# Kernel tuning notes

Measured on AMD Instinct MI355X. Metric: run time of the kernel, lower is better.

## Reference

```python
import jax, jax.numpy as jnp
import numpy as np

N_NODES = 50000
N_EDGES = 800000
F_NODE = 64
F_EDGE = 64
HIDDEN = 128


def setup_inputs() -> dict:
    key = jax.random.key(0)
    ks = jax.random.split(key, 12)
    glorot = lambda k, shape: jax.random.normal(k, shape, jnp.float32) * (2.0 / (shape[0] + shape[1])) ** 0.5
    return {
        "x": jax.random.normal(ks[0], (N_NODES, F_NODE), jnp.float32),
        "edge_index": jax.random.randint(ks[1], (2, N_EDGES), 0, N_NODES, jnp.int64),
        "edge_attr": jax.random.normal(ks[2], (N_EDGES, F_EDGE), jnp.float32),
        # edge model: MLP(concat(x_src, x_dst, edge_attr)) -> new edge_attr
        "We1": glorot(ks[3], (2 * F_NODE + F_EDGE, HIDDEN)),
        "be1": jnp.zeros((HIDDEN,), jnp.float32),
        "We2": glorot(ks[4], (HIDDEN, F_EDGE)),
        "be2": jnp.zeros((F_EDGE,), jnp.float32),
        # node model: MLP(concat(x, mean_{e: dst==i} edge_attr_e)) -> new x
        "Wn1": glorot(ks[5], (F_NODE + F_EDGE, HIDDEN)),
        "bn1": jnp.zeros((HIDDEN,), jnp.float32),
        "Wn2": glorot(ks[6], (HIDDEN, F_NODE)),
        "bn2": jnp.zeros((F_NODE,), jnp.float32),
    }


def _mlp(h, W1, b1, W2, b2):
    return jax.nn.relu(h @ W1 + b1) @ W2 + b2


def reference(x, edge_index, edge_attr, We1, be1, We2, be2, Wn1, bn1, Wn2, bn2):
    row, col = edge_index[0], edge_index[1]
    # edge model: message on each edge  [E, 2F+Fe] -> [E, Fe]
    edge_in = jnp.concatenate([x[row], x[col], edge_attr], axis=-1)
    edge_attr = _mlp(edge_in, We1, be1, We2, be2)
    # node model: mean-aggregate incoming messages at dst (col), then MLP
    agg = jax.ops.segment_sum(edge_attr, col, num_segments=N_NODES)
    cnt = jax.ops.segment_sum(jnp.ones((edge_attr.shape[0],), x.dtype), col, num_segments=N_NODES)
    agg = agg / jnp.maximum(cnt, 1.0)[:, None]
    node_in = jnp.concatenate([x, agg], axis=-1)
    x = _mlp(node_in, Wn1, bn1, Wn2, bn2)
    return (x, edge_attr)
```

## Files before the change

### kernel.cpp

```cpp
#include <hip/hip_runtime.h>


typedef __attribute__((ext_vector_type(8))) short bf16x8;
typedef __attribute__((ext_vector_type(4))) float f4;
typedef __attribute__((ext_vector_type(8))) unsigned short us8;
typedef __attribute__((ext_vector_type(4))) unsigned short us4;

constexpr int NN  = 50000;
constexpr int NE  = 800000;
constexpr int FN  = 64;
constexpr int FE  = 64;
constexpr int HID = 128;
constexpr int K1  = 2 * FN + FE;
constexpr int K2  = FN + FE;

__device__ __forceinline__ float b2f(unsigned short u) {
  union { unsigned int i; float f; } v; v.i = ((unsigned int)u) << 16; return v.f;
}
__device__ __forceinline__ unsigned short f2b(float f) {
  union { float f; unsigned int i; } v; v.f = f;
  unsigned int r = v.i + 0x7FFFu + ((v.i >> 16) & 1u);
  return (unsigned short)(r >> 16);
}
__device__ __forceinline__ void cvt16(const f4* __restrict__ p, unsigned short* dst) {
  f4 a = p[0], b = p[1], c = p[2], d = p[3];
  us8 o0, o1;
#pragma unroll
  for (int j = 0; j < 4; j++) {
    o0[j] = f2b(a[j]); o0[4 + j] = f2b(b[j]);
    o1[j] = f2b(c[j]); o1[4 + j] = f2b(d[j]);
  }
  *(us8*)dst = o0; *(us8*)(dst + 8) = o1;
}
__device__ __forceinline__ f4 MF(bf16x8 a, bf16x8 b, f4 c) {
  return __builtin_amdgcn_mfma_f32_16x16x32_bf16(a, b, c, 0, 0, 0);
}
__device__ __forceinline__ void pk_atomic_add_bf16(unsigned short* addr, unsigned int data) {
  asm volatile("global_atomic_pk_add_bf16 %0, %1, off" :: "v"(addr), "v"(data) : "memory");
}

__global__ void zeroi_kernel(unsigned int* __restrict__ p, int n) {
  int i = blockIdx.x * 256 + threadIdx.x;
  if (i < n) p[i] = 0u;
}

__global__ void cnt_kernel(const int* __restrict__ ei, float* __restrict__ cnt) {
  int e = blockIdx.x * 256 + threadIdx.x;
  if (e < NE) atomicAdd(&cnt[ei[NE + e]], 1.0f);
}

__global__ void pack_w(const float* __restrict__ W, unsigned short* __restrict__ P,
                       int N, int total) {
  int idx = blockIdx.x * 256 + threadIdx.x;
  if (idx >= total) return;
  const int l  = idx & 63;
  const int nt = (idx >> 6) % (N >> 4);
  const int s  = idx / ((N >> 4) << 6);
  const int col = nt * 16 + (l & 15);
  const int k0  = s * 32 + (l >> 4) * 8;
  us8 o;
#pragma unroll
  for (int j = 0; j < 8; j++) o[j] = f2b(W[(size_t)(k0 + j) * N + col]);
  *(us8*)(P + (size_t)idx * 8) = o;
}

__global__ __launch_bounds__(256) void edge_mlp(
    const float* __restrict__ x, const int* __restrict__ ei,
    const float* __restrict__ ea,
    const unsigned short* __restrict__ P1, const float* __restrict__ be1,
    const unsigned short* __restrict__ P2, const float* __restrict__ be2,
    float* __restrict__ eout, unsigned short* __restrict__ aggb) {
  __shared__ unsigned short sA[64][200];
  __shared__ int sC[64];
  unsigned short (*sH)[136] = (unsigned short(*)[136])&sA[0][0];
  const int tid = threadIdx.x;
  const int e0  = blockIdx.x * 64;

  {
    const int el = tid >> 2, q = tid & 3, ge = e0 + el;
    const int r = ei[ge], c = ei[NE + ge];
    if (q == 0) sC[el] = c;
    cvt16((const f4*)(x + (size_t)r * FN + q * 16), &sA[el][q * 16]);
    cvt16((const f4*)(x + (size_t)c * FN + q * 16), &sA[el][64 + q * 16]);
    cvt16((const f4*)(ea + (size_t)ge * FE + q * 16), &sA[el][128 + q * 16]);
  }
  __syncthreads();

  const int wave = tid >> 6, lane = tid & 63;
  const int mrow = lane & 15, kq = lane >> 4;

  f4 acc[4][2];
#pragma unroll
  for (int m = 0; m < 4; m++) { acc[m][0] = (f4)0.f; acc[m][1] = (f4)0.f; }
  const int nt0 = wave * 2;
#pragma unroll
  for (int s = 0; s < 6; s++) {
    bf16x8 b0 = *(const bf16x8*)(P1 + (((size_t)s * 8 + nt0)     * 64 + lane) * 8);
    bf16x8 b1 = *(const bf16x8*)(P1 + (((size_t)s * 8 + nt0 + 1) * 64 + lane) * 8);
#pragma unroll
    for (int m = 0; m < 4; m++) {
      bf16x8 a = *(const bf16x8*)&sA[m * 16 + mrow][s * 32 + kq * 8];
      acc[m][0] = MF(a, b0, acc[m][0]);
      acc[m][1] = MF(a, b1, acc[m][1]);
    }
  }
  __syncthreads();

  {
    const int c0 = nt0 * 16 + mrow, c1 = c0 + 16;
    const float bb0 = be1[c0], bb1 = be1[c1];
    const int rb = kq * 4;
#pragma unroll
    for (int m = 0; m < 4; m++)
#pragma unroll
      for (int i = 0; i < 4; i++) {
        sH[m * 16 + rb + i][c0] = f2b(fmaxf(acc[m][0][i] + bb0, 0.f));
        sH[m * 16 + rb + i][c1] = f2b(fmaxf(acc[m][1][i] + bb1, 0.f));
      }
  }
  __syncthreads();

  f4 a2[4];
#pragma unroll
  for (int m = 0; m < 4; m++) a2[m] = (f4)0.f;
#pragma unroll
  for (int s = 0; s < 4; s++) {
    bf16x8 b = *(const bf16x8*)(P2 + (((size_t)s * 4 + wave) * 64 + lane) * 8);
#pragma unroll
    for (int m = 0; m < 4; m++) {
      bf16x8 a = *(const bf16x8*)&sH[m * 16 + mrow][s * 32 + kq * 8];
      a2[m] = MF(a, b, a2[m]);
    }
  }
  {
    const int col = wave * 16 + mrow;
    const float bb = be2[col];
    const int rb = kq * 4;
    const bool even = ((lane & 1) == 0);
#pragma unroll
    for (int m = 0; m < 4; m++)
#pragma unroll
      for (int i = 0; i < 4; i++) {
        const int er = m * 16 + rb + i;
        const float v = a2[m][i] + bb;
        eout[(size_t)(e0 + er) * FE + col] = v;
        const float vp = __shfl_xor(v, 1);
        if (even) {
          const unsigned int pk =
              (unsigned int)f2b(v) | ((unsigned int)f2b(vp) << 16);
          pk_atomic_add_bf16(aggb + ((size_t)sC[er] * FE + col), pk);
        }
      }
  }
}

__global__ __launch_bounds__(256) void node_mlp(
    const float* __restrict__ x, const unsigned short* __restrict__ aggb,
    const float* __restrict__ cnt,
    const unsigned short* __restrict__ P1, const float* __restrict__ bn1,
    const unsigned short* __restrict__ P2, const float* __restrict__ bn2,
    float* __restrict__ xout) {
  __shared__ unsigned short sA[64][136];
  unsigned short (*sH)[136] = (unsigned short(*)[136])&sA[0][0];
  const int tid = threadIdx.x;
  const int n0  = blockIdx.x * 64;

  {
    const int nl = tid >> 2, q = tid & 3;
    const int gn = n0 + nl;
    if (gn < NN) {
      if (q < 2) {
        cvt16((const f4*)(x + (size_t)gn * FN + q * 32),      &sA[nl][q * 32]);
        cvt16((const f4*)(x + (size_t)gn * FN + q * 32 + 16), &sA[nl][q * 32 + 16]);
      } else {
        const float inv = 1.0f / fmaxf(cnt[gn], 1.0f);
        const int q2 = q - 2;
        const us8* pa = (const us8*)(aggb + (size_t)gn * FE + q2 * 32);
#pragma unroll
        for (int seg = 0; seg < 4; seg++) {
          us8 a = pa[seg];
          us8 o;
#pragma unroll
          for (int j = 0; j < 8; j++) o[j] = f2b(b2f(a[j]) * inv);
          *(us8*)&sA[nl][64 + q2 * 32 + seg * 8] = o;
        }
      }
    } else {
      us8 z = (us8)0;
#pragma unroll
      for (int sgi = 0; sgi < 4; sgi++) *(us8*)&sA[nl][q * 32 + sgi * 8] = z;
    }
  }
  __syncthreads();

  const int wave = tid >> 6, lane = tid & 63;
  const int mrow = lane & 15, kq = lane >> 4;

  f4 acc[4][2];
#pragma unroll
  for (int m = 0; m < 4; m++) { acc[m][0] = (f4)0.f; acc[m][1] = (f4)0.f; }
  const int nt0 = wave * 2;
#pragma unroll
  for (int s = 0; s < 4; s++) {
    bf16x8 b0 = *(const bf16x8*)(P1 + (((size_t)s * 8 + nt0)     * 64 + lane) * 8);
    bf16x8 b1 = *(const bf16x8*)(P1 + (((size_t)s * 8 + nt0 + 1) * 64 + lane) * 8);
#pragma unroll
    for (int m = 0; m < 4; m++) {
      bf16x8 a = *(const bf16x8*)&sA[m * 16 + mrow][s * 32 + kq * 8];
      acc[m][0] = MF(a, b0, acc[m][0]);
      acc[m][1] = MF(a, b1, acc[m][1]);
    }
  }
  __syncthreads();

  {
    const int c0 = nt0 * 16 + mrow, c1 = c0 + 16;
    const float bb0 = bn1[c0], bb1 = bn1[c1];
    const int rb = kq * 4;
#pragma unroll
    for (int m = 0; m < 4; m++)
#pragma unroll
      for (int i = 0; i < 4; i++) {
        sH[m * 16 + rb + i][c0] = f2b(fmaxf(acc[m][0][i] + bb0, 0.f));
        sH[m * 16 + rb + i][c1] = f2b(fmaxf(acc[m][1][i] + bb1, 0.f));
      }
  }
  __syncthreads();

  f4 a2[4];
#pragma unroll
  for (int m = 0; m < 4; m++) a2[m] = (f4)0.f;
#pragma unroll
  for (int s = 0; s < 4; s++) {
    bf16x8 b = *(const bf16x8*)(P2 + (((size_t)s * 4 + wave) * 64 + lane) * 8);
#pragma unroll
    for (int m = 0; m < 4; m++) {
      bf16x8 a = *(const bf16x8*)&sH[m * 16 + mrow][s * 32 + kq * 8];
      a2[m] = MF(a, b, a2[m]);
    }
  }
  {
    const int col = wave * 16 + mrow;
    const float bb = bn2[col];
    const int rb = kq * 4;
#pragma unroll
    for (int m = 0; m < 4; m++)
#pragma unroll
      for (int i = 0; i < 4; i++) {
        const int gn = n0 + m * 16 + rb + i;
        if (gn < NN) xout[(size_t)gn * FN + col] = a2[m][i] + bb;
      }
  }
}

extern "C" void kernel_launch(void* const* d_in, const int* in_sizes, int n_in,
                              void* d_out, int out_size, void* d_ws, size_t ws_size,
                              hipStream_t stream) {
  if (n_in != 11) return;
  if (in_sizes[0] != NN * FN) return;
  if (in_sizes[1] != 2 * NE) return;
  if (in_sizes[2] != NE * FE) return;
  if (out_size != NN * FN + NE * FE) return;
  if (ws_size < (size_t)NN * FE * 2 + (size_t)NN * 4 + 114688) return;

  const float* x   = (const float*)d_in[0];
  const int*   ei  = (const int*)d_in[1];
  const float* ea  = (const float*)d_in[2];
  const float* We1 = (const float*)d_in[3];
  const float* be1 = (const float*)d_in[4];
  const float* We2 = (const float*)d_in[5];
  const float* be2 = (const float*)d_in[6];
  const float* Wn1 = (const float*)d_in[7];
  const float* bn1 = (const float*)d_in[8];
  const float* Wn2 = (const float*)d_in[9];
  const float* bn2 = (const float*)d_in[10];

  float* xout = (float*)d_out;
  float* eout = xout + (size_t)NN * FN;

  unsigned short* aggb = (unsigned short*)d_ws;
  float* cnt = (float*)(aggb + (size_t)NN * FE);
  unsigned short* P   = (unsigned short*)(cnt + NN);
  unsigned short* Pe1 = P;
  unsigned short* Pe2 = P + 24576;
  unsigned short* Pn1 = P + 32768;
  unsigned short* Pn2 = P + 49152;

  const int zi = (NN * FE) / 2 + NN;
  zeroi_kernel<<<(zi + 255) / 256, 256, 0, stream>>>((unsigned int*)d_ws, zi);
  cnt_kernel<<<(NE + 255) / 256, 256, 0, stream>>>(ei, cnt);
  pack_w<<<(3072 + 255) / 256, 256, 0, stream>>>(We1, Pe1, HID, 3072);
  pack_w<<<(1024 + 255) / 256, 256, 0, stream>>>(We2, Pe2, FE, 1024);
  pack_w<<<(2048 + 255) / 256, 256, 0, stream>>>(Wn1, Pn1, HID, 2048);
  pack_w<<<(1024 + 255) / 256, 256, 0, stream>>>(Wn2, Pn2, FN, 1024);
  edge_mlp<<<NE / 64, 256, 0, stream>>>(x, ei, ea, Pe1, be1, Pe2, be2, eout, aggb);
  node_mlp<<<(NN + 63) / 64, 256, 0, stream>>>(x, aggb, cnt, Pn1, bn1, Pn2, bn2, xout);
}
```

Baseline: 304.7 us.

## Make edge MLP wave-independent with per-wave 16-edge tiles, removing block barriers

Each wave now owns 16 edges with its own LDS slice and computes all output column tiles itself, instead of the block sharing 64 edges across 4 waves that each compute a subset of columns. This removes the three __syncthreads barriers and replaces them with an lgkmcnt wait plus a scheduling barrier. The cost is that every wave reloads the full packed weight matrices from global memory or cache (4x more weight traffic per block), and the accumulator register count grows.

```diff
diff --git a/kernel.cpp b/kernel.cpp
--- a/kernel.cpp
+++ b/kernel.cpp
@@ -70,87 +70,84 @@
     const unsigned short* __restrict__ P1, const float* __restrict__ be1,
     const unsigned short* __restrict__ P2, const float* __restrict__ be2,
     float* __restrict__ eout, unsigned short* __restrict__ aggb) {
-  __shared__ unsigned short sA[64][200];
+  __shared__ unsigned short sW[4][16][200];
   __shared__ int sC[64];
-  unsigned short (*sH)[136] = (unsigned short(*)[136])&sA[0][0];
-  const int tid = threadIdx.x;
-  const int e0  = blockIdx.x * 64;
-
-  {
-    const int el = tid >> 2, q = tid & 3, ge = e0 + el;
+  const int tid  = threadIdx.x;
+  const int wave = tid >> 6, lane = tid & 63;
+  const int e0   = blockIdx.x * 64 + wave * 16;
+  unsigned short (*sA)[200] = sW[wave];
+  unsigned short (*sH)[136] = (unsigned short(*)[136])&sW[wave][0][0];
+
+  {
+    const int el = lane >> 2, q = lane & 3, ge = e0 + el;
     const int r = ei[ge], c = ei[NE + ge];
-    if (q == 0) sC[el] = c;
+    if (q == 0) sC[wave * 16 + el] = c;
     cvt16((const f4*)(x + (size_t)r * FN + q * 16), &sA[el][q * 16]);
     cvt16((const f4*)(x + (size_t)c * FN + q * 16), &sA[el][64 + q * 16]);
     cvt16((const f4*)(ea + (size_t)ge * FE + q * 16), &sA[el][128 + q * 16]);
   }
-  __syncthreads();
-
-  const int wave = tid >> 6, lane = tid & 63;
+
   const int mrow = lane & 15, kq = lane >> 4;
 
-  f4 acc[4][2];
-#pragma unroll
-  for (int m = 0; m < 4; m++) { acc[m][0] = (f4)0.f; acc[m][1] = (f4)0.f; }
-  const int nt0 = wave * 2;
-#pragma unroll
+  f4 acc1[8];
+#pragma unroll
+  for (int nt = 0; nt < 8; nt++) acc1[nt] = (f4)0.f;
   for (int s = 0; s < 6; s++) {
-    bf16x8 b0 = *(const bf16x8*)(P1 + (((size_t)s * 8 + nt0)     * 64 + lane) * 8);
-    bf16x8 b1 = *(const bf16x8*)(P1 + (((size_t)s * 8 + nt0 + 1) * 64 + lane) * 8);
-#pragma unroll
-    for (int m = 0; m < 4; m++) {
-      bf16x8 a = *(const bf16x8*)&sA[m * 16 + mrow][s * 32 + kq * 8];
-      acc[m][0] = MF(a, b0, acc[m][0]);
-      acc[m][1] = MF(a, b1, acc[m][1]);
-    }
-  }
-  __syncthreads();
-
-  {
-    const int c0 = nt0 * 16 + mrow, c1 = c0 + 16;
-    const float bb0 = be1[c0], bb1 = be1[c1];
-    const int rb = kq * 4;
-#pragma unroll
-    for (int m = 0; m < 4; m++)
+    bf16x8 a = *(const bf16x8*)&sA[mrow][s * 32 + kq * 8];
+#pragma unroll
+    for (int nt = 0; nt < 8; nt++) {
+      bf16x8 b = *(const bf16x8*)(P1 + (((size_t)s * 8 + nt) * 64 + lane) * 8);
+      acc1[nt] = MF(a, b, acc1[nt]);
+    }
+  }
+
+  asm volatile("s_waitcnt lgkmcnt(0)" ::: "memory");
+  __builtin_amdgcn_sched_barrier(0);
+
+  {
+    const int rb = kq * 4;
+#pragma unroll
+    for (int nt = 0; nt < 8; nt++) {
+      const int col = nt * 16 + mrow;
+      const float bb = be1[col];
+#pragma unroll
+      for (int i = 0; i < 4; i++)
+        sH[rb + i][col] = f2b(fmaxf(acc1[nt][i] + bb, 0.f));
+    }
+  }
+
+  f4 acc2[4];
+#pragma unroll
+  for (int nt = 0; nt < 4; nt++) acc2[nt] = (f4)0.f;
+  for (int s = 0; s < 4; s++) {
+    bf16x8 a = *(const bf16x8*)&sH[mrow][s * 32 + kq * 8];
+#pragma unroll
+    for (int nt = 0; nt < 4; nt++) {
+      bf16x8 b = *(const bf16x8*)(P2 + (((size_t)s * 4 + nt) * 64 + lane) * 8);
+      acc2[nt] = MF(a, b, acc2[nt]);
+    }
+  }
+
+  {
+    const int rb = kq * 4;
+    const bool even = ((lane & 1) == 0);
+#pragma unroll
+    for (int nt = 0; nt < 4; nt++) {
+      const int col = nt * 16 + mrow;
+      const float bb = be2[col];
 #pragma unroll
       for (int i = 0; i < 4; i++) {
-        sH[m * 16 + rb + i][c0] = f2b(fmaxf(acc[m][0][i] + bb0, 0.f));
-        sH[m * 16 + rb + i][c1] = f2b(fmaxf(acc[m][1][i] + bb1, 0.f));
-      }
-  }
-  __syncthreads();
-
-  f4 a2[4];
-#pragma unroll
-  for (int m = 0; m < 4; m++) a2[m] = (f4)0.f;
-#pragma unroll
-  for (int s = 0; s < 4; s++) {
-    bf16x8 b = *(const bf16x8*)(P2 + (((size_t)s * 4 + wave) * 64 + lane) * 8);
-#pragma unroll
-    for (int m = 0; m < 4; m++) {
-      bf16x8 a = *(const bf16x8*)&sH[m * 16 + mrow][s * 32 + kq * 8];
-      a2[m] = MF(a, b, a2[m]);
-    }
-  }
-  {
-    const int col = wave * 16 + mrow;
-    const float bb = be2[col];
-    const int rb = kq * 4;
-    const bool even = ((lane & 1) == 0);
-#pragma unroll
-    for (int m = 0; m < 4; m++)
-#pragma unroll
-      for (int i = 0; i < 4; i++) {
-        const int er = m * 16 + rb + i;
-        const float v = a2[m][i] + bb;
-        eout[(size_t)(e0 + er) * FE + col] = v;
+        const int erl = rb + i;
+        const float v = acc2[nt][i] + bb;
+        eout[(size_t)(e0 + erl) * FE + col] = v;
         const float vp = __shfl_xor(v, 1);
         if (even) {
           const unsigned int pk =
               (unsigned int)f2b(v) | ((unsigned int)f2b(vp) << 16);
-          pk_atomic_add_bf16(aggb + ((size_t)sC[er] * FE + col), pk);
+          pk_atomic_add_bf16(aggb + ((size_t)sC[wave * 16 + erl] * FE + col), pk);
         }
       }
+    }
   }
 }
 
```

New measurement: 361.9 us. 1.19x slower.

## Make edge MLP persistent with register-prefetched gathers for the next tile

Applied to the files above, without the earlier changes.

The edge kernel now runs a fixed grid of 2500 blocks, each handling 5 tiles of 64 edges. While the MFMA work for the current tile runs, the x/edge_attr gathers for the next tile and the edge indices for the tile after that are loaded into registers. This hides gather latency behind compute and cuts block launch overhead. The cost is higher register pressure, which can lower occupancy, and fewer blocks to spread across CUs.

```diff
diff --git a/kernel.cpp b/kernel.cpp
--- a/kernel.cpp
+++ b/kernel.cpp
@@ -4,7 +4,6 @@
 typedef __attribute__((ext_vector_type(8))) short bf16x8;
 typedef __attribute__((ext_vector_type(4))) float f4;
 typedef __attribute__((ext_vector_type(8))) unsigned short us8;
-typedef __attribute__((ext_vector_type(4))) unsigned short us4;
 
 constexpr int NN  = 50000;
 constexpr int NE  = 800000;
@@ -13,6 +12,8 @@
 constexpr int HID = 128;
 constexpr int K1  = 2 * FN + FE;
 constexpr int K2  = FN + FE;
+constexpr int GRID_E    = 2500;
+constexpr int TPB_TILES = 5;
 
 __device__ __forceinline__ float b2f(unsigned short u) {
   union { unsigned int i; float f; } v; v.i = ((unsigned int)u) << 16; return v.f;
@@ -22,15 +23,22 @@
   unsigned int r = v.i + 0x7FFFu + ((v.i >> 16) & 1u);
   return (unsigned short)(r >> 16);
 }
+__device__ __forceinline__ void st16(const f4* r, unsigned short* dst) {
+  us8 o0, o1;
+#pragma unroll
+  for (int j = 0; j < 4; j++) {
+    o0[j] = f2b(r[0][j]); o0[4 + j] = f2b(r[1][j]);
+    o1[j] = f2b(r[2][j]); o1[4 + j] = f2b(r[3][j]);
+  }
+  *(us8*)dst = o0; *(us8*)(dst + 8) = o1;
+}
+__device__ __forceinline__ void ld16(const float* p, f4* r) {
+  const f4* pp = (const f4*)p;
+  r[0] = pp[0]; r[1] = pp[1]; r[2] = pp[2]; r[3] = pp[3];
+}
 __device__ __forceinline__ void cvt16(const f4* __restrict__ p, unsigned short* dst) {
-  f4 a = p[0], b = p[1], c = p[2], d = p[3];
-  us8 o0, o1;
-#pragma unroll
-  for (int j = 0; j < 4; j++) {
-    o0[j] = f2b(a[j]); o0[4 + j] = f2b(b[j]);
-    o1[j] = f2b(c[j]); o1[4 + j] = f2b(d[j]);
-  }
-  *(us8*)dst = o0; *(us8*)(dst + 8) = o1;
+  f4 r[4] = {p[0], p[1], p[2], p[3]};
+  st16(r, dst);
 }
 __device__ __forceinline__ f4 MF(bf16x8 a, bf16x8 b, f4 c) {
   return __builtin_amdgcn_mfma_f32_16x16x32_bf16(a, b, c, 0, 0, 0);
@@ -73,84 +81,118 @@
   __shared__ unsigned short sA[64][200];
   __shared__ int sC[64];
   unsigned short (*sH)[136] = (unsigned short(*)[136])&sA[0][0];
-  const int tid = threadIdx.x;
-  const int e0  = blockIdx.x * 64;
-
-  {
-    const int el = tid >> 2, q = tid & 3, ge = e0 + el;
-    const int r = ei[ge], c = ei[NE + ge];
-    if (q == 0) sC[el] = c;
-    cvt16((const f4*)(x + (size_t)r * FN + q * 16), &sA[el][q * 16]);
-    cvt16((const f4*)(x + (size_t)c * FN + q * 16), &sA[el][64 + q * 16]);
-    cvt16((const f4*)(ea + (size_t)ge * FE + q * 16), &sA[el][128 + q * 16]);
-  }
-  __syncthreads();
-
+  const int tid  = threadIdx.x;
   const int wave = tid >> 6, lane = tid & 63;
   const int mrow = lane & 15, kq = lane >> 4;
-
-  f4 acc[4][2];
-#pragma unroll
-  for (int m = 0; m < 4; m++) { acc[m][0] = (f4)0.f; acc[m][1] = (f4)0.f; }
-  const int nt0 = wave * 2;
-#pragma unroll
-  for (int s = 0; s < 6; s++) {
-    bf16x8 b0 = *(const bf16x8*)(P1 + (((size_t)s * 8 + nt0)     * 64 + lane) * 8);
-    bf16x8 b1 = *(const bf16x8*)(P1 + (((size_t)s * 8 + nt0 + 1) * 64 + lane) * 8);
-#pragma unroll
-    for (int m = 0; m < 4; m++) {
-      bf16x8 a = *(const bf16x8*)&sA[m * 16 + mrow][s * 32 + kq * 8];
-      acc[m][0] = MF(a, b0, acc[m][0]);
-      acc[m][1] = MF(a, b1, acc[m][1]);
-    }
-  }
-  __syncthreads();
+  const int el = tid >> 2, q = tid & 3;
+
+  f4 rx0[4], rx1[4], rea[4];
+  int rN, cN;
+  int cStage;
 
   {
-    const int c0 = nt0 * 16 + mrow, c1 = c0 + 16;
-    const float bb0 = be1[c0], bb1 = be1[c1];
-    const int rb = kq * 4;
-#pragma unroll
-    for (int m = 0; m < 4; m++)
-#pragma unroll
-      for (int i = 0; i < 4; i++) {
-        sH[m * 16 + rb + i][c0] = f2b(fmaxf(acc[m][0][i] + bb0, 0.f));
-        sH[m * 16 + rb + i][c1] = f2b(fmaxf(acc[m][1][i] + bb1, 0.f));
-      }
-  }
-  __syncthreads();
-
-  f4 a2[4];
-#pragma unroll
-  for (int m = 0; m < 4; m++) a2[m] = (f4)0.f;
-#pragma unroll
-  for (int s = 0; s < 4; s++) {
-    bf16x8 b = *(const bf16x8*)(P2 + (((size_t)s * 4 + wave) * 64 + lane) * 8);
-#pragma unroll
-    for (int m = 0; m < 4; m++) {
-      bf16x8 a = *(const bf16x8*)&sH[m * 16 + mrow][s * 32 + kq * 8];
-      a2[m] = MF(a, b, a2[m]);
-    }
-  }
-  {
-    const int col = wave * 16 + mrow;
-    const float bb = be2[col];
-    const int rb = kq * 4;
-    const bool even = ((lane & 1) == 0);
-#pragma unroll
-    for (int m = 0; m < 4; m++)
-#pragma unroll
-      for (int i = 0; i < 4; i++) {
-        const int er = m * 16 + rb + i;
-        const float v = a2[m][i] + bb;
-        eout[(size_t)(e0 + er) * FE + col] = v;
-        const float vp = __shfl_xor(v, 1);
-        if (even) {
-          const unsigned int pk =
-              (unsigned int)f2b(v) | ((unsigned int)f2b(vp) << 16);
-          pk_atomic_add_bf16(aggb + ((size_t)sC[er] * FE + col), pk);
+    const int ge = blockIdx.x * 64 + el;
+    const int r = ei[ge], c = ei[NE + ge];
+    cStage = c;
+    ld16(x + (size_t)r * FN + q * 16, rx0);
+    ld16(x + (size_t)c * FN + q * 16, rx1);
+    ld16(ea + (size_t)ge * FE + q * 16, rea);
+    const int ge1 = (blockIdx.x + GRID_E) * 64 + el;
+    rN = ei[ge1];
+    cN = ei[NE + ge1];
+  }
+
+  for (int j = 0; j < TPB_TILES; j++) {
+    const int e0 = (blockIdx.x + j * GRID_E) * 64;
+    __syncthreads();
+
+    {
+      if (q == 0) sC[el] = cStage;
+      st16(rx0, &sA[el][q * 16]);
+      st16(rx1, &sA[el][64 + q * 16]);
+      st16(rea, &sA[el][128 + q * 16]);
+    }
+    __syncthreads();
+
+    if (j + 1 < TPB_TILES) {
+      const int rr = rN, cc = cN;
+      cStage = cc;
+      const int geN = e0 + GRID_E * 64 + el;
+      ld16(x + (size_t)rr * FN + q * 16, rx0);
+      ld16(x + (size_t)cc * FN + q * 16, rx1);
+      ld16(ea + (size_t)geN * FE + q * 16, rea);
+      if (j + 2 < TPB_TILES) {
+        const int ge2 = e0 + 2 * GRID_E * 64 + el;
+        rN = ei[ge2];
+        cN = ei[NE + ge2];
+      }
+    }
+    __builtin_amdgcn_sched_barrier(0);
+
+    f4 acc[4][2];
+#pragma unroll
+    for (int m = 0; m < 4; m++) { acc[m][0] = (f4)0.f; acc[m][1] = (f4)0.f; }
+    const int nt0 = wave * 2;
+#pragma unroll
+    for (int s = 0; s < 6; s++) {
+      bf16x8 b0 = *(const bf16x8*)(P1 + (((size_t)s * 8 + nt0)     * 64 + lane) * 8);
+      bf16x8 b1 = *(const bf16x8*)(P1 + (((size_t)s * 8 + nt0 + 1) * 64 + lane) * 8);
+#pragma unroll
+      for (int m = 0; m < 4; m++) {
+        bf16x8 a = *(const bf16x8*)&sA[m * 16 + mrow][s * 32 + kq * 8];
+        acc[m][0] = MF(a, b0, acc[m][0]);
+        acc[m][1] = MF(a, b1, acc[m][1]);
+      }
+    }
+    __syncthreads();
+
+    {
+      const int c0 = nt0 * 16 + mrow, c1 = c0 + 16;
+      const float bb0 = be1[c0], bb1 = be1[c1];
+      const int rb = kq * 4;
+#pragma unroll
+      for (int m = 0; m < 4; m++)
+#pragma unroll
+        for (int i = 0; i < 4; i++) {
+          sH[m * 16 + rb + i][c0] = f2b(fmaxf(acc[m][0][i] + bb0, 0.f));
+          sH[m * 16 + rb + i][c1] = f2b(fmaxf(acc[m][1][i] + bb1, 0.f));
         }
-      }
+    }
+    __syncthreads();
+
+    f4 a2[4];
+#pragma unroll
+    for (int m = 0; m < 4; m++) a2[m] = (f4)0.f;
+#pragma unroll
+    for (int s = 0; s < 4; s++) {
+      bf16x8 b = *(const bf16x8*)(P2 + (((size_t)s * 4 + wave) * 64 + lane) * 8);
+#pragma unroll
+      for (int m = 0; m < 4; m++) {
+        bf16x8 a = *(const bf16x8*)&sH[m * 16 + mrow][s * 32 + kq * 8];
+        a2[m] = MF(a, b, a2[m]);
+      }
+    }
+
+    {
+      const int col = wave * 16 + mrow;
+      const float bb = be2[col];
+      const int rb = kq * 4;
+      const bool even = ((lane & 1) == 0);
+#pragma unroll
+      for (int m = 0; m < 4; m++)
+#pragma unroll
+        for (int i = 0; i < 4; i++) {
+          const int er = m * 16 + rb + i;
+          const float v = a2[m][i] + bb;
+          eout[(size_t)(e0 + er) * FE + col] = v;
+          const float vp = __shfl_xor(v, 1);
+          if (even) {
+            const unsigned int pk =
+                (unsigned int)f2b(v) | ((unsigned int)f2b(vp) << 16);
+            pk_atomic_add_bf16(aggb + ((size_t)sC[er] * FE + col), pk);
+          }
+        }
+    }
   }
 }
 
@@ -293,6 +335,6 @@
   pack_w<<<(1024 + 255) / 256, 256, 0, stream>>>(We2, Pe2, FE, 1024);
   pack_w<<<(2048 + 255) / 256, 256, 0, stream>>>(Wn1, Pn1, HID, 2048);
   pack_w<<<(1024 + 255) / 256, 256, 0, stream>>>(Wn2, Pn2, FN, 1024);
-  edge_mlp<<<NE / 64, 256, 0, stream>>>(x, ei, ea, Pe1, be1, Pe2, be2, eout, aggb);
+  edge_mlp<<<GRID_E, 256, 0, stream>>>(x, ei, ea, Pe1, be1, Pe2, be2, eout, aggb);
   node_mlp<<<(NN + 63) / 64, 256, 0, stream>>>(x, aggb, cnt, Pn1, bn1, Pn2, bn2, xout);
 }
```

Result: faster. 279.3 us (-8.3%).
